# Kernel optimization log

Measured on AMD Instinct MI355X. Metric: run time of the kernel, lower is better.

Reference implementation:

```python
import jax, jax.numpy as jnp
import numpy as np

N, D_IN, D_OUT = 16384, 64, 64
AVG_DEG = 32.0
L2_EPS = 1e-12  # torch F.normalize default eps


def setup_inputs() -> dict:
    key = jax.random.key(0)
    kx, ka, kw, kb = jax.random.split(key, 4)
    X = jax.random.normal(kx, (N, D_IN), dtype=jnp.float32)
    # binary adjacency with avg degree ~AVG_DEG (module treats adj as 0/1 mask)
    adj = (jax.random.uniform(ka, (N, N)) < (AVG_DEG / N)).astype(jnp.float32)
    # nn.Linear(2*D_IN, D_OUT): store W as (2*D_IN, D_OUT) for x @ W + b
    bound = 1.0 / np.sqrt(2 * D_IN)
    W = jax.random.uniform(kw, (2 * D_IN, D_OUT), dtype=jnp.float32, minval=-bound, maxval=bound)
    b = jax.random.uniform(kb, (D_OUT,), dtype=jnp.float32, minval=-bound, maxval=bound)
    return {"X": X, "adj": adj, "W": W, "b": b}


def reference(X, adj, W, b):
    # eval-mode mean aggregation: h_neigh = (adj + I) @ X / clamp(rowsum(adj + I), 1)
    # (adj + I) @ X == adj @ X + X, avoiding materializing the NxN identity.
    deg = jnp.clip(jnp.sum(adj, axis=1, keepdims=True) + 1.0, 1.0, None)  # (N,1)
    h_neigh = (adj @ X + X) / deg                                          # (N,D)
    concat = jnp.concatenate([X, h_neigh], axis=1)                         # (N,2D)
    z = concat @ W + b                                                     # (N,O)
    out = jax.nn.relu(z)
    norm = jnp.linalg.norm(out, axis=1, keepdims=True)
    return out / jnp.maximum(norm, L2_EPS)
```

## Files before the change

### kernel.cpp

```cpp
#include <hip/hip_runtime.h>
#include <stdint.h>


#define NROWS   16384
#define DDIM    64
#define MAXNNZ  256
#define NBLOCKS 4096

typedef uint32_t u32x4 __attribute__((ext_vector_type(4)));

__global__ __launch_bounds__(256, 4) void sage_fused(
    const float* __restrict__ X,
    const float* __restrict__ adj,
    const float* __restrict__ W,
    const float* __restrict__ bias,
    float* __restrict__ out)
{
    __shared__ int   slist[4][MAXNNZ];
    __shared__ int   scnt[4];
    __shared__ float scat[4][2 * DDIM];

    const int tid  = threadIdx.x;
    const int lane = tid & 63;
    const int w    = tid >> 6;
    const int row  = blockIdx.x * 4 + w;

    const float bv = bias[lane];

    if (lane == 0) scnt[w] = 0;
    __builtin_amdgcn_wave_barrier();

    const int start = (row * 7 + (row >> 4)) & 15;
    const u32x4* rowp = reinterpret_cast<const u32x4*>(adj + (size_t)row * NROWS);

    u32x4 buf[2][4];
    {
        const int ss0 = start;
        const int ss1 = (start + 1) & 15;
#pragma unroll
        for (int q = 0; q < 4; ++q)
            buf[0][q] = __builtin_nontemporal_load(&rowp[ss0 * 256 + q * 64 + lane]);
#pragma unroll
        for (int q = 0; q < 4; ++q)
            buf[1][q] = __builtin_nontemporal_load(&rowp[ss1 * 256 + q * 64 + lane]);
    }

#pragma unroll 2
    for (int s = 0; s < 16; ++s) {
        const int cur = s & 1;
        const int ss  = (s + start) & 15;
#pragma unroll
        for (int q = 0; q < 4; ++q) {
            const u32x4 vv = buf[cur][q];
            if (vv.x | vv.y | vv.z | vv.w) {
                const int base = (ss * 256 + q * 64 + lane) * 4;
                const uint32_t w4[4] = { vv.x, vv.y, vv.z, vv.w };
#pragma unroll
                for (int j = 0; j < 4; ++j) {
                    if (w4[j]) {
                        const int p = atomicAdd(&scnt[w], 1);
                        if (p < MAXNNZ) slist[w][p] = base + j;
                    }
                }
            }
        }
        if (s < 14) {
            const int ssn = (s + 2 + start) & 15;
#pragma unroll
            for (int q = 0; q < 4; ++q)
                buf[cur][q] = __builtin_nontemporal_load(&rowp[ssn * 256 + q * 64 + lane]);
        }
    }
    __builtin_amdgcn_wave_barrier();

    const int nnz = scnt[w];
    const int cn  = (nnz < MAXNNZ) ? nnz : MAXNNZ;

    float acc = 0.0f;
    int k = 0;
    for (; k + 4 <= cn; k += 4) {
        const int j0 = slist[w][k], j1 = slist[w][k + 1];
        const int j2 = slist[w][k + 2], j3 = slist[w][k + 3];
        const float a0 = X[(size_t)j0 * DDIM + lane];
        const float a1 = X[(size_t)j1 * DDIM + lane];
        const float a2 = X[(size_t)j2 * DDIM + lane];
        const float a3 = X[(size_t)j3 * DDIM + lane];
        acc += (a0 + a1) + (a2 + a3);
    }
    for (; k < cn; ++k) acc += X[(size_t)slist[w][k] * DDIM + lane];

    const float xi = X[(size_t)row * DDIM + lane];
    const float h  = (acc + xi) / ((float)nnz + 1.0f);
    scat[w][lane]        = xi;
    scat[w][DDIM + lane] = h;
    __builtin_amdgcn_wave_barrier();

    float z0 = bv, z1 = 0.0f, z2 = 0.0f, z3 = 0.0f;
#pragma unroll 8
    for (int kk = 0; kk < 2 * DDIM; kk += 4) {
        z0 = fmaf(scat[w][kk + 0], W[(kk + 0) * DDIM + lane], z0);
        z1 = fmaf(scat[w][kk + 1], W[(kk + 1) * DDIM + lane], z1);
        z2 = fmaf(scat[w][kk + 2], W[(kk + 2) * DDIM + lane], z2);
        z3 = fmaf(scat[w][kk + 3], W[(kk + 3) * DDIM + lane], z3);
    }
    float z = (z0 + z1) + (z2 + z3);
    z = fmaxf(z, 0.0f);

    float s2 = z * z;
#pragma unroll
    for (int off = 32; off >= 1; off >>= 1) s2 += __shfl_xor(s2, off);
    const float inv = 1.0f / fmaxf(sqrtf(s2), 1e-12f);
    out[(size_t)row * DDIM + lane] = z * inv;
}

extern "C" void kernel_launch(void* const* d_in, const int* in_sizes, int n_in,
                              void* d_out, int out_size, void* d_ws, size_t ws_size,
                              hipStream_t stream) {
    const float* X   = (const float*)d_in[0];
    const float* adj = (const float*)d_in[1];
    const float* W   = (const float*)d_in[2];
    const float* b   = (const float*)d_in[3];
    float* out = (float*)d_out;
    sage_fused<<<NBLOCKS, 256, 0, stream>>>(X, adj, W, b, out);
}
```

Baseline: 1.292 ms.

## Split adjacency scan into grid-strided kernel writing per-row neighbor lists

Replaces the per-row fused scan with a separate kernel that streams the whole adjacency matrix with a flat grid-stride loop. It appends column indices to per-row lists in workspace using global atomics. A second kernel then gathers X rows, applies the linear layer and normalizes. The aim is more uniform, higher-bandwidth streaming of the 1 GB adjacency matrix. The cost is global atomics, an extra memset and launch, and neighbor lists capped at 128 per row.

```diff
diff --git a/kernel.cpp b/kernel.cpp
--- a/kernel.cpp
+++ b/kernel.cpp
@@ -5,9 +5,112 @@
 #define NROWS   16384
 #define DDIM    64
 #define MAXNNZ  256
+#define MAXN    128
 #define NBLOCKS 4096
+#define SCAN_TPB    256
+#define SCAN_BLOCKS 2048
 
 typedef uint32_t u32x4 __attribute__((ext_vector_type(4)));
+
+__device__ __forceinline__ void proc_vec(u32x4 v, int vi,
+                                         int* __restrict__ cnt,
+                                         int* __restrict__ list) {
+    if (v.x | v.y | v.z | v.w) {
+        const uint32_t wd[4] = { v.x, v.y, v.z, v.w };
+#pragma unroll
+        for (int j = 0; j < 4; ++j) {
+            if (wd[j]) {
+                const int e = vi * 4 + j;
+                const int r = e >> 14;
+                const int c = e & (NROWS - 1);
+                const int p = atomicAdd(&cnt[r], 1);
+                if (p < MAXN) list[(size_t)r * MAXN + p] = c;
+            }
+        }
+    }
+}
+
+__global__ __launch_bounds__(SCAN_TPB, 4) void adj_scan(
+    const float* __restrict__ adj,
+    int* __restrict__ cnt,
+    int* __restrict__ list)
+{
+    const u32x4* p = reinterpret_cast<const u32x4*>(adj);
+    const int stride = SCAN_BLOCKS * SCAN_TPB;
+    int i = blockIdx.x * SCAN_TPB + threadIdx.x;
+    for (int it = 0; it < 32; ++it) {
+        const int i0 = i;
+        const int i1 = i + stride;
+        const int i2 = i + 2 * stride;
+        const int i3 = i + 3 * stride;
+        const u32x4 v0 = __builtin_nontemporal_load(&p[i0]);
+        const u32x4 v1 = __builtin_nontemporal_load(&p[i1]);
+        const u32x4 v2 = __builtin_nontemporal_load(&p[i2]);
+        const u32x4 v3 = __builtin_nontemporal_load(&p[i3]);
+        proc_vec(v0, i0, cnt, list);
+        proc_vec(v1, i1, cnt, list);
+        proc_vec(v2, i2, cnt, list);
+        proc_vec(v3, i3, cnt, list);
+        i += 4 * stride;
+    }
+}
+
+__global__ __launch_bounds__(256, 4) void sage_agg(
+    const float* __restrict__ X,
+    const int*   __restrict__ cnt,
+    const int*   __restrict__ list,
+    const float* __restrict__ W,
+    const float* __restrict__ bias,
+    float* __restrict__ out)
+{
+    __shared__ float scat[4][2 * DDIM];
+
+    const int tid  = threadIdx.x;
+    const int lane = tid & 63;
+    const int w    = tid >> 6;
+    const int row  = blockIdx.x * 4 + w;
+
+    const float bv = bias[lane];
+
+    const int nnz = cnt[row];
+    const int cn  = (nnz < MAXN) ? nnz : MAXN;
+    const int* lp = list + (size_t)row * MAXN;
+
+    float acc = 0.0f;
+    int k = 0;
+    for (; k + 4 <= cn; k += 4) {
+        const int j0 = lp[k], j1 = lp[k + 1], j2 = lp[k + 2], j3 = lp[k + 3];
+        const float a0 = X[(size_t)j0 * DDIM + lane];
+        const float a1 = X[(size_t)j1 * DDIM + lane];
+        const float a2 = X[(size_t)j2 * DDIM + lane];
+        const float a3 = X[(size_t)j3 * DDIM + lane];
+        acc += (a0 + a1) + (a2 + a3);
+    }
+    for (; k < cn; ++k) acc += X[(size_t)lp[k] * DDIM + lane];
+
+    const float xi = X[(size_t)row * DDIM + lane];
+    const float h  = (acc + xi) / ((float)nnz + 1.0f);
+    scat[w][lane]        = xi;
+    scat[w][DDIM + lane] = h;
+    __builtin_amdgcn_wave_barrier();
+
+    float z0 = bv, z1 = 0.0f, z2 = 0.0f, z3 = 0.0f;
+#pragma unroll 8
+    for (int kk = 0; kk < 2 * DDIM; kk += 4) {
+        z0 = fmaf(scat[w][kk + 0], W[(kk + 0) * DDIM + lane], z0);
+        z1 = fmaf(scat[w][kk + 1], W[(kk + 1) * DDIM + lane], z1);
+        z2 = fmaf(scat[w][kk + 2], W[(kk + 2) * DDIM + lane], z2);
+        z3 = fmaf(scat[w][kk + 3], W[(kk + 3) * DDIM + lane], z3);
+    }
+    float z = (z0 + z1) + (z2 + z3);
+    z = fmaxf(z, 0.0f);
+
+    float s2 = z * z;
+#pragma unroll
+    for (int off = 32; off >= 1; off >>= 1) s2 += __shfl_xor(s2, off);
+    const float inv = 1.0f / fmaxf(sqrtf(s2), 1e-12f);
+    out[(size_t)row * DDIM + lane] = z * inv;
+}
 
 __global__ __launch_bounds__(256, 4) void sage_fused(
     const float* __restrict__ X,
@@ -121,5 +224,16 @@
     const float* W   = (const float*)d_in[2];
     const float* b   = (const float*)d_in[3];
     float* out = (float*)d_out;
-    sage_fused<<<NBLOCKS, 256, 0, stream>>>(X, adj, W, b, out);
-}
+
+    const size_t need = (size_t)NROWS * sizeof(int)
+                      + (size_t)NROWS * MAXN * sizeof(int);
+    if (d_ws != nullptr && ws_size >= need) {
+        int* cnt  = (int*)d_ws;
+        int* list = cnt + NROWS;
+        hipMemsetAsync(cnt, 0, (size_t)NROWS * sizeof(int), stream);
+        adj_scan<<<SCAN_BLOCKS, SCAN_TPB, 0, stream>>>(adj, cnt, list);
+        sage_agg<<<NBLOCKS, 256, 0, stream>>>(X, cnt, list, W, b, out);
+    } else {
+        sage_fused<<<NBLOCKS, 256, 0, stream>>>(X, adj, W, b, out);
+    }
+}
```

Result: slower. 1.362 ms (+5.4%).
